# Optimization experiments

Hardware: AMD Instinct MI355X
Metric: run time of the kernel (lower is better)

## Reference

```python
import jax, jax.numpy as jnp
import numpy as np

B, C, H, W = 8, 256, 96, 96
HEADS, WS = 8, 12
HD = C // HEADS
SCALE = HD ** -0.5
L = WS * WS  # tokens per window


def _rel_index(ws):
    # Swin-style relative position index, computed statically (matches torch.meshgrid 'ij')
    coords = np.stack(np.meshgrid(np.arange(ws), np.arange(ws), indexing='ij')).reshape(2, -1)
    rel = (coords[:, :, None] - coords[:, None, :]).transpose(1, 2, 0) + (ws - 1)
    return rel[..., 0] * (2 * ws - 1) + rel[..., 1]  # [L, L]

REL_IDX = jnp.asarray(_rel_index(WS).reshape(-1))


def dct1(x):
    # 1D DCT-II along last axis via rfft, matches the torch implementation
    n = x.shape[-1]
    xv = jnp.concatenate([x, x[..., ::-1]], axis=-1)
    X = jnp.fft.rfft(xv, axis=-1)[..., :n]
    k = jnp.arange(n, dtype=jnp.float32)
    Wc = jnp.exp(-1j * jnp.pi * k / (2 * n))
    return (X * Wc).real.astype(jnp.float32)


def dct2(x):
    x = dct1(x.swapaxes(-1, -2)).swapaxes(-1, -2)
    return dct1(x)


def idct1(X):
    n = X.shape[-1]
    k = jnp.arange(n, dtype=jnp.float32)
    Wc = jnp.exp(1j * jnp.pi * k / (2 * n))
    Xc = X.astype(jnp.complex64) * Wc
    Xc_full = jnp.concatenate([Xc, Xc[..., 1:-1][..., ::-1]], axis=-1)
    # irfft with n=2n crops input to n+1 bins, exactly like torch.fft.irfft
    x = jnp.fft.irfft(Xc_full, n=2 * n, axis=-1)
    return x[..., :n].astype(jnp.float32)


def idct2(x):
    x = idct1(x.swapaxes(-1, -2)).swapaxes(-1, -2)
    return idct1(x)


def conv2d(x, w, groups=1, pad=0):
    return jax.lax.conv_general_dilated(
        x, w, (1, 1), [(pad, pad), (pad, pad)],
        dimension_numbers=('NCHW', 'OIHW', 'NCHW'), feature_group_count=groups)


def batchnorm(x, g, b):
    # training-mode BN (module default): per-batch statistics over (B,H,W)
    m = x.mean(axis=(0, 2, 3), keepdims=True)
    v = x.var(axis=(0, 2, 3), keepdims=True)
    return (x - m) * jax.lax.rsqrt(v + 1e-5) * g.reshape(1, -1, 1, 1) + b.reshape(1, -1, 1, 1)


def setup_inputs() -> dict:
    key = jax.random.key(0)
    ks = jax.random.split(key, 10)
    def rn(k, shape, s=0.02):
        return jax.random.normal(k, shape, dtype=jnp.float32) * s
    return {
        'x': jax.random.normal(ks[0], (B, C, H, W), dtype=jnp.float32),
        'qkv_w': rn(ks[1], (3 * C, C)), 'qkv_b': jnp.zeros((3 * C,), jnp.float32),
        'proj_w': rn(ks[2], (C, C)), 'proj_b': jnp.zeros((C,), jnp.float32),
        'lpe_w': rn(ks[3], (C, 1, 3, 3), 0.1), 'lpe_b': jnp.zeros((C,), jnp.float32),
        'lpe_scale': jnp.ones((1,), jnp.float32),
        'rpb_table': rn(ks[4], ((2 * WS - 1) ** 2, HEADS), 0.02),
        'ec_w': rn(ks[5], (1, 1, 3, 3), 0.3),
        'bn1_g': jnp.ones((1,), jnp.float32), 'bn1_b': jnp.zeros((1,), jnp.float32),
        'nl_w': rn(ks[6], (1, 1), 1.0), 'nl_b': jnp.zeros((1,), jnp.float32),
        'fr_w': rn(ks[7], (C, C, 1, 1), 0.05),
        'bn2_g': jnp.ones((C,), jnp.float32), 'bn2_b': jnp.zeros((C,), jnp.float32),
    }


def reference(x, qkv_w, qkv_b, proj_w, proj_b, lpe_w, lpe_b, lpe_scale, rpb_table,
              ec_w, bn1_g, bn1_b, nl_w, nl_b, fr_w, bn2_g, bn2_b):
    # ---- FreqNoiseDetector ----
    freq = jnp.abs(dct2(x))                                      # [B,C,H,W]
    mn = freq.min(axis=(2, 3), keepdims=True)
    mx = freq.max(axis=(2, 3), keepdims=True)
    freq_norm = (freq - mn) / (mx + 1e-6)
    local_energy = jax.nn.relu(batchnorm(
        conv2d(freq_norm.mean(axis=1, keepdims=True), ec_w, pad=1), bn1_g, bn1_b))  # [B,1,H,W]
    pooled = local_energy.mean(axis=(2, 3))                      # [B,1]
    noise_global = jax.nn.sigmoid(pooled @ nl_w.T + nl_b)        # [B,1]
    noise_mask = jax.nn.sigmoid(1.0 - local_energy) * noise_global.reshape(B, 1, 1, 1)

    # ---- DynamicAttention: SW-MSA with relative position bias ----
    xh = x.transpose(0, 2, 3, 1)                                 # [B,H,W,C]
    win = xh.reshape(B, H // WS, WS, W // WS, WS, C).transpose(0, 1, 3, 2, 4, 5).reshape(-1, L, C)
    qkv = (win @ qkv_w.T + qkv_b).reshape(-1, L, 3, HEADS, HD).transpose(2, 0, 3, 1, 4)
    q, k, v = qkv[0], qkv[1], qkv[2]                             # [Bw,h,L,hd]
    attn = jnp.einsum('bhld,bhmd->bhlm', q, k) * SCALE
    bias = rpb_table[REL_IDX].reshape(L, L, HEADS).transpose(2, 0, 1)
    attn = jax.nn.softmax(attn + bias[None], axis=-1)
    out = jnp.einsum('bhlm,bhmd->bhld', attn, v).transpose(0, 2, 1, 3).reshape(-1, L, C)
    out = out @ proj_w.T + proj_b
    x_attn = out.reshape(B, H // WS, W // WS, WS, WS, C).transpose(0, 1, 3, 2, 4, 5).reshape(B, H, W, C)
    # noise-guided depthwise LPE
    x_lpe = (conv2d(x, lpe_w, groups=C, pad=1) + lpe_b.reshape(1, C, 1, 1)) * lpe_scale * noise_mask
    x_attn_img = x_attn.transpose(0, 3, 1, 2) + x_lpe            # [B,C,H,W]

    # ---- frequency soft gate ----
    freq2 = dct2(x_attn_img)
    freq_mean = freq2.mean(axis=(2, 3), keepdims=True)
    gate = jax.nn.sigmoid(5.0 * (jnp.abs(freq2) - freq_mean))
    x_freq = idct2(freq2 * gate)

    # ---- 1x1 refine + residual ----
    y = batchnorm(conv2d(x + x_freq, fr_w), bn2_g, bn2_b)
    return jax.nn.gelu(y, approximate=False)
```

## Files before the change

### kernel.cpp

```cpp
#include <hip/hip_runtime.h>
#include <math.h>

#define Bb     8
#define Cc     256
#define Hh     96
#define Ww     96
#define HEADS  8
#define WS_    12
#define HD     32
#define LL     144
#define NPIX   9216
#define NPLANE 2048
#define NTOK   73728
#define NWIN   512
#define SCALE_ 0.17677669529663687f
#define BN1N   73728.0f
#define GELC   0.7071067811865476f

#define OFF_DT    0
#define OFF_FNM   18432
#define OFF_E     92160
#define OFF_MASK  165888
#define OFF_P3    239616
#define OFF_ST1   240192
#define OFF_BN2   240200
#define OFF_BUF0  262144
#define OFF_BUF1  19136512
#define OFF_BUF2  38010880

#define QKV_TSEC 4718592

typedef short bf16x8 __attribute__((ext_vector_type(8)));
typedef short s16x4  __attribute__((ext_vector_type(4)));
typedef float f32x4  __attribute__((ext_vector_type(4)));

static __device__ __forceinline__ float sigm(float x){ return 1.0f/(1.0f+__expf(-x)); }

static __device__ __forceinline__ void split2(float f, short& h, short& l){
  unsigned u = __float_as_uint(f);
  unsigned hb = u & 0xffff0000u;
  h = (short)(hb>>16);
  float lo = f - __uint_as_float(hb);
  l = (short)(__float_as_uint(lo)>>16);
}

__global__ void k_mat(short* DFh, short* DFl, short* MFh, short* MFl){
  int t = blockIdx.x*256 + threadIdx.x;
  int m = t/9216, u = t - m*9216;
  int k = u/96, n = u - k*96;
  double v;
  if (m == 0){
    v = 2.0*cos(3.14159265358979323846*(double)n*(double)(2*k+1)/192.0);
  } else {
    v = (k==0) ? 1.0 : 2.0*cos(3.14159265358979323846*(double)k*(double)(2*n+1)/192.0);
    if (k == 94) v += cos(3.14159265358979323846*94.0/192.0) * ((n&1)? -1.0 : 1.0);
    v /= 192.0;
  }
  float f = (float)v;
  short hs, ls; split2(f, hs, ls);
  int kt = k>>5, lr = (k>>3)&3, jj = k&7, nt = n>>4;
  int idx = ((kt*6+nt)*64 + (lr*16 + (n&15)))*8 + jj;
  if (m == 0){ DFh[idx]=hs; DFl[idx]=ls; }
  else       { MFh[idx]=hs; MFl[idx]=ls; }
}

__global__ __launch_bounds__(256) void k_plane(const float* __restrict__ in, float* __restrict__ out,
                                               const short* __restrict__ Fh, const short* __restrict__ Fl,
                                               int mode){
  __shared__ __align__(16) short Xh[96*104];
  __shared__ __align__(16) short Xl[96*104];
  __shared__ float red[512];
  const int tid = threadIdx.x;
  const int lane = tid & 63, wid = tid >> 6;
  const int l15 = lane & 15, l4 = lane >> 4;
  const float* src = in + (size_t)blockIdx.x*NPIX;

  for (int t4 = tid; t4 < 576; t4 += 256){
    int rt = t4/24, ct = t4 - rt*24;
    const float* p0 = src + rt*4*96 + ct*4;
    float4 v0 = *(const float4*)(p0);
    float4 v1 = *(const float4*)(p0+96);
    float4 v2 = *(const float4*)(p0+192);
    float4 v3 = *(const float4*)(p0+288);
#define STCOL(f0,f1,f2,f3,j) { s16x4 hv, lv; short hs, ls; \
    split2(f0,hs,ls); hv[0]=hs; lv[0]=ls; \
    split2(f1,hs,ls); hv[1]=hs; lv[1]=ls; \
    split2(f2,hs,ls); hv[2]=hs; lv[2]=ls; \
    split2(f3,hs,ls); hv[3]=hs; lv[3]=ls; \
    int cc = ct*4+(j); \
    *(s16x4*)&Xh[cc*104 + rt*4] = hv; \
    *(s16x4*)&Xl[cc*104 + rt*4] = lv; }
    STCOL(v0.x,v1.x,v2.x,v3.x,0)
    STCOL(v0.y,v1.y,v2.y,v3.y,1)
    STCOL(v0.z,v1.z,v2.z,v3.z,2)
    STCOL(v0.w,v1.w,v2.w,v3.w,3)
#undef STCOL
  }
  __syncthreads();

  f32x4 acc[9];
  #pragma unroll
  for (int t=0;t<9;++t) acc[t] = (f32x4){0.f,0.f,0.f,0.f};

  #pragma unroll
  for (int t=0;t<9;++t){
    int gt = wid*9 + t;
    int mt = gt/6, nt = gt - mt*6;
    int arow = mt*16 + l15;
    #pragma unroll
    for (int kb=0;kb<3;++kb){
      bf16x8 ah = *(const bf16x8*)&Xh[arow*104 + kb*32 + l4*8];
      bf16x8 al = *(const bf16x8*)&Xl[arow*104 + kb*32 + l4*8];
      const bf16x8 bh = *(const bf16x8*)(Fh + (size_t)((kb*6+nt)*64 + lane)*8);
      const bf16x8 bl = *(const bf16x8*)(Fl + (size_t)((kb*6+nt)*64 + lane)*8);
      acc[t] = __builtin_amdgcn_mfma_f32_16x16x32_bf16(al, bh, acc[t], 0,0,0);
      acc[t] = __builtin_amdgcn_mfma_f32_16x16x32_bf16(ah, bl, acc[t], 0,0,0);
      acc[t] = __builtin_amdgcn_mfma_f32_16x16x32_bf16(ah, bh, acc[t], 0,0,0);
    }
  }
  __syncthreads();

  #pragma unroll
  for (int t=0;t<9;++t){
    int gt = wid*9 + t;
    int mt = gt/6, nt = gt - mt*6;
    int ti = nt*16 + l15, tj = mt*16 + l4*4;
    s16x4 hv, lv; short hs, ls;
    split2(acc[t][0],hs,ls); hv[0]=hs; lv[0]=ls;
    split2(acc[t][1],hs,ls); hv[1]=hs; lv[1]=ls;
    split2(acc[t][2],hs,ls); hv[2]=hs; lv[2]=ls;
    split2(acc[t][3],hs,ls); hv[3]=hs; lv[3]=ls;
    *(s16x4*)&Xh[ti*104+tj] = hv;
    *(s16x4*)&Xl[ti*104+tj] = lv;
  }
  #pragma unroll
  for (int t=0;t<9;++t) acc[t] = (f32x4){0.f,0.f,0.f,0.f};
  __syncthreads();

  #pragma unroll
  for (int t=0;t<9;++t){
    int gt = wid*9 + t;
    int it = gt/6, jt = gt - it*6;
    int arow = it*16 + l15;
    #pragma unroll
    for (int kb=0;kb<3;++kb){
      bf16x8 ah = *(const bf16x8*)&Xh[arow*104 + kb*32 + l4*8];
// ... 58 lines not shown
      int i0 = it*16 + l4*4, j = jt*16 + l15;
      #pragma unroll
      for (int p=0;p<4;++p){
        float v = acc[t][p];
        dst[(i0+p)*96 + j] = v * sigm(5.f*(fabsf(v)-mean));
      }
    }
  }
}

__global__ void k_chmean(const float* __restrict__ A, float* __restrict__ FNM){
  int px = blockIdx.x*256 + threadIdx.x;
  int b = px/NPIX, p = px - b*NPIX;
  const float* base = A + (size_t)b*Cc*NPIX + p;
  float s = 0.f;
  #pragma unroll 8
  for (int c=0;c<Cc;++c) s += base[(size_t)c*NPIX];
  FNM[px] = s*(1.f/256.f);
}

__global__ void k_conv3(const float* __restrict__ FNM, const float* __restrict__ w9,
                        float* __restrict__ E, float* __restrict__ P3){
  __shared__ float rs[256], rq[256];
  int px = blockIdx.x*256 + threadIdx.x;
  int b = px/NPIX, p = px - b*NPIX;
  int h = p/96, w = p - h*96;
  const float* base = FNM + b*NPIX;
  float a = 0.f;
  #pragma unroll
  for (int dy=0;dy<3;++dy){
    int hh = h+dy-1;
    if (hh>=0 && hh<96){
      #pragma unroll
      for (int dx=0;dx<3;++dx){
        int ww2 = w+dx-1;
        if (ww2>=0 && ww2<96) a = fmaf(base[hh*96+ww2], w9[dy*3+dx], a);
      }
    }
  }
  E[px] = a;
  rs[threadIdx.x]=a; rq[threadIdx.x]=a*a; __syncthreads();
  for (int o=128;o;o>>=1){
    if (threadIdx.x<o){ rs[threadIdx.x]+=rs[threadIdx.x+o]; rq[threadIdx.x]+=rq[threadIdx.x+o]; }
    __syncthreads();
  }
  if (threadIdx.x==0){ P3[2*blockIdx.x]=rs[0]; P3[2*blockIdx.x+1]=rq[0]; }
}

__global__ void k_red576(const float* __restrict__ P3, float* __restrict__ ST1){
  __shared__ float rs[256], rq[256];
  float s=0.f,q=0.f;
  for (int i=threadIdx.x;i<288;i+=256){ s+=P3[2*i]; q+=P3[2*i+1]; }
  rs[threadIdx.x]=s; rq[threadIdx.x]=q; __syncthreads();
  for (int o=128;o;o>>=1){
    if (threadIdx.x<o){ rs[threadIdx.x]+=rs[threadIdx.x+o]; rq[threadIdx.x]+=rq[threadIdx.x+o]; }
    __syncthreads();
  }
  if (threadIdx.x==0){ ST1[0]=rs[0]; ST1[1]=rq[0]; }
}

__global__ void k_mask(const float* __restrict__ E, const float* __restrict__ ST1,
                       const float* __restrict__ g1, const float* __restrict__ b1,
                       const float* __restrict__ nw, const float* __restrict__ nb,
                       float* __restrict__ MASK){
  __shared__ float les[NPIX];
  __shared__ float red[256];
  int b = blockIdx.x, tid = threadIdx.x;
  float m = ST1[0]*(1.f/BN1N);
  float v = ST1[1]*(1.f/BN1N) - m*m;
  float rstd = rsqrtf(v + 1e-5f);
  float ga = g1[0], be = b1[0];
  float local = 0.f;
  for (int p=tid;p<NPIX;p+=256){
    float le = fmaxf(0.f, (E[b*NPIX+p]-m)*rstd*ga + be);
    les[p] = le; local += le;
  }
  red[tid]=local; __syncthreads();
  for (int o=128;o;o>>=1){ if (tid<o) red[tid]+=red[tid+o]; __syncthreads(); }
  float ng = sigm(red[0]*(1.f/9216.f)*nw[0] + nb[0]);
  for (int p=tid;p<NPIX;p+=256)
    MASK[b*NPIX+p] = sigm(1.f - les[p]) * ng;
}

__global__ void k_tr(const float* __restrict__ x, float* __restrict__ XT){
  __shared__ float tile[32][33];
  int pt = blockIdx.x*32, ct = blockIdx.y*32, b = blockIdx.z;
  int txd = threadIdx.x, tyd = threadIdx.y;
  #pragma unroll
  for (int q=0;q<4;++q){
    int c = ct + tyd + q*8;
    tile[tyd+q*8][txd] = x[(size_t)(b*Cc+c)*NPIX + pt + txd];
  }
  __syncthreads();
  #pragma unroll
  for (int q=0;q<4;++q){
    int p = pt + tyd + q*8;
    XT[(size_t)(b*NPIX+p)*Cc + ct + txd] = tile[txd][tyd+q*8];
  }
}

__global__ __launch_bounds__(256) void k_qkv(const float* __restrict__ XT, const float* __restrict__ Wq,
                                             const float* __restrict__ bq, float* __restrict__ qkv, int g){
  __shared__ __align__(16) float As[16*128];
  __shared__ __align__(16) float Bs[16*96];
  const int mt = blockIdx.x, nt = blockIdx.y;
  const int r0 = mt*128;
  const int tid = threadIdx.x;
  const int ty = tid>>4, tx = tid&15;
  float acc[8][6];
  #pragma unroll
  for (int a=0;a<8;++a){
    #pragma unroll
    for (int b=0;b<6;++b) acc[a][b]=0.f;
  }

  for (int k0=0;k0<256;k0+=16){
    #pragma unroll
    for (int it=0;it<2;++it){
      int f = tid + it*256;
      int i = f>>2, kq = f&3;
      int r = r0 + i;
      int win = r/144, l = r - win*144;
      int b = win>>6, wh = (win>>3)&7, wwi = win&7;
      int lh = l/12, lw = l - lh*12;
      int pix = (wh*12+lh)*96 + wwi*12+lw;
      float4 v = *(const float4*)&XT[((size_t)((b*NPIX)+pix))*256 + k0 + (kq<<2)];
      int kk = kq<<2;
      As[(kk+0)*128+i]=v.x; As[(kk+1)*128+i]=v.y; As[(kk+2)*128+i]=v.z; As[(kk+3)*128+i]=v.w;
    }
    #pragma unroll
    for (int it=0;it<2;++it){
      int f = tid + it*256;
      if (f < 384){
        int c = f>>2, kq = f&3;
        int cg = nt*96 + c;
        int t = cg>>6, hl = (cg>>5)&1, d = cg&31;
        int wrow = t*256 + (g*2+hl)*32 + d;
        float4 v = *(const float4*)&Wq[(size_t)wrow*256 + k0 + (kq<<2)];
        int kk = kq<<2;
        Bs[(kk+0)*96+c]=v.x; Bs[(kk+1)*96+c]=v.y; Bs[(kk+2)*96+c]=v.z; Bs[(kk+3)*96+c]=v.w;
      }
    }
    __syncthreads();
    #pragma unroll
    for (int k=0;k<16;++k){
      const float4* pa = (const float4*)&As[k*128 + ty*8];
      float4 a0 = pa[0], a1 = pa[1];
      float av[8] = {a0.x,a0.y,a0.z,a0.w,a1.x,a1.y,a1.z,a1.w};
      const float2* pb = (const float2*)&Bs[k*96];
      float2 b0 = pb[tx], b1 = pb[tx+16], b2 = pb[tx+32];
      float bv[6] = {b0.x,b0.y,b1.x,b1.y,b2.x,b2.y};
      #pragma unroll
      for (int ii=0;ii<8;++ii){
        #pragma unroll
        for (int jj=0;jj<6;++jj) acc[ii][jj] = fmaf(av[ii], bv[jj], acc[ii][jj]);
      }
    }
    __syncthreads();
  }
  #pragma unroll
  for (int ii=0;ii<8;++ii){
    int r = r0 + ty*8 + ii;
    int win = r/144, l = r - win*144;
    #pragma unroll
    for (int jj=0;jj<6;++jj){
      int s = jj>>1;
      int c = nt*96 + 2*tx + s*32 + (jj&1);
      int t = c>>6, hl = (c>>5)&1, d = c&31;
      float val = acc[ii][jj] + bq[t*256 + (g*2+hl)*32 + d];
      qkv[(size_t)t*QKV_TSEC + ((size_t)(win*2+hl)*144 + l)*32 + d] = val;
    }
  }
}

__global__ __launch_bounds__(192) void k_attn(const float* __restrict__ qkv, const float* __restrict__ rpb,
                                              float* __restrict__ O, int g){
  __shared__ __align__(16) float qt[32*144];
  __shared__ __align__(16) float Ks[144*32];
  __shared__ __align__(16) float Vs[144*32];
  __shared__ float rpbs[532];
  const int win = blockIdx.x, hl = blockIdx.y;
  const int head = g*2 + hl;
  const int tid = threadIdx.x;
  const float* Qg = qkv + ((size_t)(win*2+hl)*144)*32;
  const float* Kg = Qg + QKV_TSEC;
  const float* Vg = Qg + 2*(size_t)QKV_TSEC;
  for (int t=tid; t<4608; t+=192){
    Ks[t] = Kg[t]; Vs[t] = Vg[t];
    int l = t>>5, d = t&31;
    qt[d*144+l] = Qg[t];
  }
  for (int t=tid; t<529; t+=192) rpbs[t] = rpb[t*8 + head];
  __syncthreads();

  int r = tid;
  if (r < 144){
    float q[32];
    #pragma unroll
    for (int d=0;d<32;++d) q[d] = qt[d*144+r];
    float o[32];
    #pragma unroll
    for (int d=0;d<32;++d) o[d]=0.f;
    float m = -3.4e38f, sum = 0.f;
    int rh = r/12, rw = r - rh*12;
    int jh = 0, jw = 0;
    for (int j=0;j<144;++j){
      const float4* kp = (const float4*)&Ks[j*32];
      float s0=0,s1=0,s2=0,s3=0;
      #pragma unroll
      for (int t=0;t<8;++t){
        float4 kv = kp[t];
        s0 = fmaf(q[4*t+0],kv.x,s0); s1 = fmaf(q[4*t+1],kv.y,s1);
        s2 = fmaf(q[4*t+2],kv.z,s2); s3 = fmaf(q[4*t+3],kv.w,s3);
      }
      float s = ((s0+s1)+(s2+s3))*SCALE_ + rpbs[(rh-jh+11)*23 + (rw-jw+11)];
      float mn2 = fmaxf(m, s);
      if (mn2 > m){
        float corr = __expf(m - mn2);
        sum *= corr;
        #pragma unroll
        for (int d=0;d<32;++d) o[d]*=corr;
        m = mn2;
      }
      float p = __expf(s - m);
      sum += p;
      const float4* vp = (const float4*)&Vs[j*32];
      #pragma unroll
      for (int t=0;t<8;++t){
        float4 vv = vp[t];
        o[4*t+0]=fmaf(p,vv.x,o[4*t+0]); o[4*t+1]=fmaf(p,vv.y,o[4*t+1]);
        o[4*t+2]=fmaf(p,vv.z,o[4*t+2]); o[4*t+3]=fmaf(p,vv.w,o[4*t+3]);
      }
      if (++jw==12){ jw=0; ++jh; }
    }
    float inv = 1.f/sum;
    float* dst = O + ((size_t)(win*144+r))*256 + head*32;
    #pragma unroll
    for (int t=0;t<8;++t){
      float4 t4 = { o[4*t]*inv, o[4*t+1]*inv, o[4*t+2]*inv, o[4*t+3]*inv };
      *(float4*)&dst[4*t] = t4;
    }
  }
}

__global__ void k_lpe(const float* __restrict__ x, const float* __restrict__ lw,
                      const float* __restrict__ lb, const float* __restrict__ ls,
                      const float* __restrict__ MASK, float* __restrict__ Y1){
  float scale = ls[0];
  for (size_t idx = (size_t)blockIdx.x*256 + threadIdx.x; idx < (size_t)Bb*Cc*NPIX; idx += (size_t)gridDim.x*256){
    int pc = (int)(idx/NPIX); int p = (int)(idx - (size_t)pc*NPIX);
    int b = pc>>8, c = pc&255;
    int h = p/96, w = p - h*96;
    const float* xp = x + (size_t)pc*NPIX;
    const float* wp = lw + c*9;
    float a = 0.f;
    #pragma unroll
    for (int dy=0;dy<3;++dy){
      int hh = h+dy-1;
      if (hh>=0 && hh<96){
        #pragma unroll
        for (int dx=0;dx<3;++dx){
          int ww2 = w+dx-1;
          if (ww2>=0 && ww2<96) a = fmaf(xp[hh*96+ww2], wp[dy*3+dx], a);
        }
      }
    }
    Y1[idx] += (a + lb[c]) * scale * MASK[b*NPIX+p];
  }
}

__global__ __launch_bounds__(256) void k_proj(const float* __restrict__ O, const float* __restrict__ Wp,
                                              const float* __restrict__ bp, float* __restrict__ PROJ){
  __shared__ __align__(16) float As[16*128];
  __shared__ __align__(16) float Bs[16*128];
  const int mt = blockIdx.x, nt = blockIdx.y;
  const int r0 = mt*128, c0 = nt*128;
  const int tid = threadIdx.x;
  const int ty = tid>>4, tx = tid&15;
  float acc[8][8];
  #pragma unroll
  for (int a=0;a<8;++a){
    #pragma unroll
    for (int b=0;b<8;++b) acc[a][b]=0.f;
  }

  for (int k0=0;k0<256;k0+=16){
    #pragma unroll
    for (int it=0;it<2;++it){
      int f = tid + it*256;
      int i = f>>2, kq = f&3;
      float4 v = *(const float4*)&O[((size_t)(r0+i))*256 + k0 + (kq<<2)];
      int kk = kq<<2;
      As[(kk+0)*128+i]=v.x; As[(kk+1)*128+i]=v.y; As[(kk+2)*128+i]=v.z; As[(kk+3)*128+i]=v.w;
    }
    #pragma unroll
    for (int it=0;it<2;++it){
      int f = tid + it*256;
      int c = f>>2, kq = f&3;
      float4 v = *(const float4*)&Wp[((size_t)(c0+c))*256 + k0 + (kq<<2)];
      int kk = kq<<2;
      Bs[(kk+0)*128+c]=v.x; Bs[(kk+1)*128+c]=v.y; Bs[(kk+2)*128+c]=v.z; Bs[(kk+3)*128+c]=v.w;
    }
    __syncthreads();
    #pragma unroll
    for (int k=0;k<16;++k){
      const float4* pa = (const float4*)&As[k*128 + ty*8];
      float4 a0 = pa[0], a1 = pa[1];
      float av[8] = {a0.x,a0.y,a0.z,a0.w,a1.x,a1.y,a1.z,a1.w};
      const float4* pb = (const float4*)&Bs[k*128];
      float4 b0 = pb[tx], b1 = pb[tx+16];
      float bv[8] = {b0.x,b0.y,b0.z,b0.w,b1.x,b1.y,b1.z,b1.w};
      #pragma unroll
      for (int ii=0;ii<8;++ii){
        #pragma unroll
        for (int jj=0;jj<8;++jj) acc[ii][jj] = fmaf(av[ii], bv[jj], acc[ii][jj]);
      }
    }
    __syncthreads();
  }
  const float4 bp0 = *(const float4*)&bp[c0 + 4*tx];
  const float4 bp1 = *(const float4*)&bp[c0 + 64 + 4*tx];
  #pragma unroll
  for (int ii=0;ii<8;++ii){
    int r = r0 + ty*8 + ii;
    float* pp = PROJ + (size_t)r*256 + c0;
    float4 v0 = { acc[ii][0]+bp0.x, acc[ii][1]+bp0.y, acc[ii][2]+bp0.z, acc[ii][3]+bp0.w };
    float4 v1 = { acc[ii][4]+bp1.x, acc[ii][5]+bp1.y, acc[ii][6]+bp1.z, acc[ii][7]+bp1.w };
    *(float4*)&pp[4*tx] = v0;
    *(float4*)&pp[64 + 4*tx] = v1;
  }
}

__global__ __launch_bounds__(256) void k_merge(const float* __restrict__ PROJ, float* __restrict__ Y1){
  __shared__ float T[96*65];
  const int bx = blockIdx.x;
  const int b = bx/96, h = bx - b*96;
  const int wh = h/12, lh = h - wh*12;
  const int c0 = blockIdx.y*64;
  const int t = threadIdx.x;
  const int wave = t>>6, lane = t&63;
  for (int it=0; it<24; ++it){
    int tok = wave*24 + it;
    int wwi = tok/12, lw = tok - wwi*12;
    int gtok = (b*64 + wh*8 + wwi)*144 + lh*12 + lw;
    T[tok*65 + lane] = PROJ[(size_t)gtok*256 + c0 + lane];
  }
  __syncthreads();
  const int cl = t>>2, p0 = (t&3)*24;
  float* dst = Y1 + ((size_t)(b*Cc + c0 + cl))*NPIX + h*96 + p0;
  #pragma unroll
  for (int i=0;i<24;i+=4){
    float4 v = { T[(p0+i)*65+cl], T[(p0+i+1)*65+cl], T[(p0+i+2)*65+cl], T[(p0+i+3)*65+cl] };
    *(float4*)&dst[i] = v;
  }
}

__global__ __launch_bounds__(256) void k_conv1x1(const float* __restrict__ x, const float* __restrict__ XF,
                                                 const float* __restrict__ Wf, float* __restrict__ Z){
  __shared__ __align__(16) float As[16*128];
  __shared__ __align__(16) float Bs[16*128];
  const int mt = blockIdx.x, nt = blockIdx.y;
  const int gp0 = mt*128;
  const int b = gp0/NPIX, p0 = gp0 - b*NPIX;
  const int c0 = nt*128;
  const int tid = threadIdx.x;
  const int ty = tid>>4, tx = tid&15;
  float acc[8][8];
  #pragma unroll
  for (int a=0;a<8;++a){
    #pragma unroll
    for (int bb=0;bb<8;++bb) acc[a][bb]=0.f;
  }

  for (int k0=0;k0<256;k0+=16){
    #pragma unroll
    for (int it=0;it<2;++it){
      int f = tid + it*256;
      int k = f>>5, i4 = f&31;
      size_t off = ((size_t)(b*Cc + k0 + k))*NPIX + p0 + i4*4;
      float4 va = *(const float4*)&x[off];
      float4 vb = *(const float4*)&XF[off];
      float4 s = { va.x+vb.x, va.y+vb.y, va.z+vb.z, va.w+vb.w };
      *(float4*)&As[k*128 + i4*4] = s;
    }
    #pragma unroll
    for (int it=0;it<2;++it){
      int f = tid + it*256;
      int c = f>>2, kq = f&3;
      float4 v = *(const float4*)&Wf[((size_t)(c0+c))*256 + k0 + (kq<<2)];
      int kk = kq<<2;
      Bs[(kk+0)*128+c]=v.x; Bs[(kk+1)*128+c]=v.y; Bs[(kk+2)*128+c]=v.z; Bs[(kk+3)*128+c]=v.w;
    }
    __syncthreads();
    #pragma unroll
    for (int k=0;k<16;++k){
      const float4* pa = (const float4*)&As[k*128 + ty*8];
      float4 a0 = pa[0], a1 = pa[1];
      float av[8] = {a0.x,a0.y,a0.z,a0.w,a1.x,a1.y,a1.z,a1.w};
      const float4* pb = (const float4*)&Bs[k*128];
      float4 b0 = pb[tx], b1 = pb[tx+16];
      float bv[8] = {b0.x,b0.y,b0.z,b0.w,b1.x,b1.y,b1.z,b1.w};
      #pragma unroll
      for (int ii=0;ii<8;++ii){
        #pragma unroll
        for (int jj=0;jj<8;++jj) acc[ii][jj] = fmaf(av[ii], bv[jj], acc[ii][jj]);
      }
    }
    __syncthreads();
  }
  #pragma unroll
  for (int jj=0;jj<8;++jj){
    int co = c0 + ((jj<4)? 4*tx+jj : 64 + 4*tx + (jj-4));
    float4 lo = {acc[0][jj],acc[1][jj],acc[2][jj],acc[3][jj]};
    float4 hi = {acc[4][jj],acc[5][jj],acc[6][jj],acc[7][jj]};
    float* zp = Z + ((size_t)(b*Cc+co))*NPIX + p0 + ty*8;
    *(float4*)zp = lo;
    *(float4*)(zp+4) = hi;
  }
}

__global__ void k_bnstat(const float* __restrict__ Z, float* __restrict__ BN2){
  __shared__ float rs[256], rq[256];
  int c = blockIdx.x, tid = threadIdx.x;
  float s=0.f,q=0.f;
  for (int b=0;b<Bb;++b){
    const float* pl = Z + ((size_t)(b*Cc+c))*NPIX;
    for (int i=tid;i<NPIX/4;i+=256){
      float4 v = *(const float4*)&pl[i*4];
      s += v.x+v.y+v.z+v.w;
      q += v.x*v.x + v.y*v.y + v.z*v.z + v.w*v.w;
    }
  }
  rs[tid]=s; rq[tid]=q; __syncthreads();
  for (int o=128;o;o>>=1){
    if (tid<o){ rs[tid]+=rs[tid+o]; rq[tid]+=rq[tid+o]; }
    __syncthreads();
  }
  if (tid==0){ BN2[c]=rs[0]; BN2[256+c]=rq[0]; }
}

__global__ void k_final(const float* __restrict__ Z, const float* __restrict__ BN2,
                        const float* __restrict__ g2, const float* __restrict__ b2,
                        float* __restrict__ out){
  size_t f4 = (size_t)blockIdx.x*256 + threadIdx.x;
  size_t base = f4*4;
  int c = (int)((base/NPIX) & 255);
  float m = BN2[c]*(1.f/BN1N);
  float v = BN2[256+c]*(1.f/BN1N) - m*m;
  float rstd = rsqrtf(v+1e-5f);
  float ga = g2[c], be = b2[c];
  float4 z = *(const float4*)&Z[base];
  float4 r;
  float y;
  y = (z.x-m)*rstd*ga + be; r.x = 0.5f*y*(1.f+erff(y*GELC));
  y = (z.y-m)*rstd*ga + be; r.y = 0.5f*y*(1.f+erff(y*GELC));
  y = (z.z-m)*rstd*ga + be; r.z = 0.5f*y*(1.f+erff(y*GELC));
  y = (z.w-m)*rstd*ga + be; r.w = 0.5f*y*(1.f+erff(y*GELC));
  *(float4*)&out[base] = r;
}

extern "C" void kernel_launch(void* const* d_in, const int* in_sizes, int n_in,
                              void* d_out, int out_size, void* d_ws, size_t ws_size,
                              hipStream_t stream){
  const float* x      = (const float*)d_in[0];
  const float* qkv_w  = (const float*)d_in[1];
  const float* qkv_b  = (const float*)d_in[2];
  const float* proj_w = (const float*)d_in[3];
  const float* proj_b = (const float*)d_in[4];
  const float* lpe_w  = (const float*)d_in[5];
  const float* lpe_b  = (const float*)d_in[6];
  const float* lpe_s  = (const float*)d_in[7];
  const float* rpb    = (const float*)d_in[8];
  const float* ec_w   = (const float*)d_in[9];
  const float* bn1_g  = (const float*)d_in[10];
  const float* bn1_b  = (const float*)d_in[11];
  const float* nl_w   = (const float*)d_in[12];
  const float* nl_b   = (const float*)d_in[13];
  const float* fr_w   = (const float*)d_in[14];
  const float* bn2_g  = (const float*)d_in[15];
  const float* bn2_b  = (const float*)d_in[16];
  float* outp = (float*)d_out;

  float* WS   = (float*)d_ws;
  short* FR   = (short*)(WS + OFF_DT);
  short* DFh  = FR;
  short* DFl  = FR + 9216;
  short* MFh  = FR + 18432;
  short* MFl  = FR + 27648;
  float* FNM  = WS + OFF_FNM;
  float* E    = WS + OFF_E;
  float* MASK = WS + OFF_MASK;
  float* P3   = WS + OFF_P3;
  float* ST1  = WS + OFF_ST1;
  float* BN2  = WS + OFF_BN2;
  float* BUF0 = WS + OFF_BUF0;
  float* BUF1 = WS + OFF_BUF1;
  float* BUF2 = WS + OFF_BUF2;

  k_mat<<<72,256,0,stream>>>(DFh, DFl, MFh, MFl);
  k_plane<<<NPLANE,256,0,stream>>>(x, BUF2, DFh, DFl, 0);
  k_chmean<<<288,256,0,stream>>>(BUF2, FNM);
  k_conv3<<<288,256,0,stream>>>(FNM, ec_w, E, P3);
  k_red576<<<1,256,0,stream>>>(P3, ST1);
  k_mask<<<8,256,0,stream>>>(E, ST1, bn1_g, bn1_b, nl_w, nl_b, MASK);
  k_tr<<<dim3(288,8,8),dim3(32,8),0,stream>>>(x, BUF0);
  for (int g=0; g<4; ++g){
    k_qkv<<<dim3(576,2),256,0,stream>>>(BUF0, qkv_w, qkv_b, BUF1, g);
    k_attn<<<dim3(512,2),192,0,stream>>>(BUF1, rpb, BUF2, g);
  }
  k_proj<<<dim3(576,2),256,0,stream>>>(BUF2, proj_w, proj_b, BUF0);
  k_merge<<<dim3(768,4),256,0,stream>>>(BUF0, BUF1);
  k_lpe<<<4096,256,0,stream>>>(x, lpe_w, lpe_b, lpe_s, MASK, BUF1);
  k_plane<<<NPLANE,256,0,stream>>>(BUF1, BUF2, DFh, DFl, 1);
  k_plane<<<NPLANE,256,0,stream>>>(BUF2, BUF0, MFh, MFl, 2);
  k_conv1x1<<<dim3(576,2),256,0,stream>>>(x, BUF0, fr_w, BUF1);
  k_bnstat<<<256,256,0,stream>>>(BUF1, BN2);
  k_final<<<18432,256,0,stream>>>(BUF1, BN2, bn2_g, bn2_b, outp);
}
```

Before: 1.828 ms.

## Move QKV, projection and 1x1 conv GEMMs to split-bf16 MFMA; fuse LPE into merge

Replaces the three FP32 SIMT GEMMs (QKV, output projection, 1x1 refine conv) with MFMA bf16 kernels that use a hi/lo split (three MFMAs per tile) to keep near-FP32 accuracy. Weights are pre-swizzled into MFMA fragment layout, and activations are split into bf16 pairs at the producer: the transpose now writes window-ordered tokens, and attention writes split output. The depthwise LPE conv is folded into the merge kernel, which removes a separate pass over the full tensor. Buffers are reused heavily, which risks aliasing mistakes, and the split costs some accuracy and extra operand traffic.

```diff
diff --git a/kernel.cpp b/kernel.cpp
--- a/kernel.cpp
+++ b/kernel.cpp
@@ -3,8 +3,6 @@
 
 #define Bb     8
 #define Cc     256
-#define Hh     96
-#define Ww     96
 #define HEADS  8
 #define WS_    12
 #define HD     32
@@ -29,6 +27,8 @@
 #define OFF_BUF2  38010880
 
 #define QKV_TSEC 4718592
+#define QF_OFF  14155776
+#define PF_OFF  14352384
 
 typedef short bf16x8 __attribute__((ext_vector_type(8)));
 typedef short s16x4  __attribute__((ext_vector_type(4)));
@@ -62,6 +62,31 @@
   int idx = ((kt*6+nt)*64 + (lr*16 + (n&15)))*8 + jj;
   if (m == 0){ DFh[idx]=hs; DFl[idx]=ls; }
   else       { MFh[idx]=hs; MFl[idx]=ls; }
+}
+
+__global__ void k_wfrag(const float* __restrict__ qw, const float* __restrict__ pw,
+                        short* QFh, short* QFl, short* PFh, short* PFl){
+  int t = blockIdx.x*256 + threadIdx.x;
+  if (t < 196608){
+    int wrow = t>>8, k = t&255;
+    int sec = wrow>>8, rem = wrow&255, head = rem>>5, d = rem&31;
+    int g = head>>1, hl = head&1;
+    int nl = sec*64 + hl*32 + d;
+    int idx = (((g*8 + (k>>5))*12 + (nl>>4))*64 + ((k>>3)&3)*16 + (nl&15))*8 + (k&7);
+    short h,l; split2(qw[t],h,l); QFh[idx]=h; QFl[idx]=l;
+  } else {
+    int u = t - 196608;
+    int n = u>>8, k = u&255;
+    int idx = (((k>>5)*16 + (n>>4))*64 + ((k>>3)&3)*16 + (n&15))*8 + (k&7);
+    short h,l; split2(pw[u],h,l); PFh[idx]=h; PFl[idx]=l;
+  }
+}
+
+__global__ void k_wfrag_fr(const float* __restrict__ fw, short* FFh, short* FFl){
+  int u = blockIdx.x*256 + threadIdx.x;
+  int n = u>>8, k = u&255;
+  int idx = (((k>>5)*16 + (n>>4))*64 + ((k>>3)&3)*16 + (n&15))*8 + (k&7);
+  short h,l; split2(fw[u],h,l); FFh[idx]=h; FFl[idx]=l;
 }
 
 __global__ __launch_bounds__(256) void k_plane(const float* __restrict__ in, float* __restrict__ out,
@@ -286,7 +311,7 @@
     MASK[b*NPIX+p] = sigm(1.f - les[p]) * ng;
 }
 
-__global__ void k_tr(const float* __restrict__ x, float* __restrict__ XT){
+__global__ void k_tr(const float* __restrict__ x, short* __restrict__ XTH, short* __restrict__ XTL){
   __shared__ float tile[32][33];
   int pt = blockIdx.x*32, ct = blockIdx.y*32, b = blockIdx.z;
   int txd = threadIdx.x, tyd = threadIdx.y;
@@ -299,86 +324,69 @@
   #pragma unroll
   for (int q=0;q<4;++q){
     int p = pt + tyd + q*8;
-    XT[(size_t)(b*NPIX+p)*Cc + ct + txd] = tile[txd][tyd+q*8];
-  }
-}
-
-__global__ __launch_bounds__(256) void k_qkv(const float* __restrict__ XT, const float* __restrict__ Wq,
-                                             const float* __restrict__ bq, float* __restrict__ qkv, int g){
-  __shared__ __align__(16) float As[16*128];
-  __shared__ __align__(16) float Bs[16*96];
-  const int mt = blockIdx.x, nt = blockIdx.y;
-  const int r0 = mt*128;
-  const int tid = threadIdx.x;
-  const int ty = tid>>4, tx = tid&15;
-  float acc[8][6];
-  #pragma unroll
-  for (int a=0;a<8;++a){
-    #pragma unroll
-    for (int b=0;b<6;++b) acc[a][b]=0.f;
-  }
-
-  for (int k0=0;k0<256;k0+=16){
-    #pragma unroll
-    for (int it=0;it<2;++it){
-      int f = tid + it*256;
-      int i = f>>2, kq = f&3;
-      int r = r0 + i;
-      int win = r/144, l = r - win*144;
-      int b = win>>6, wh = (win>>3)&7, wwi = win&7;
-      int lh = l/12, lw = l - lh*12;
-      int pix = (wh*12+lh)*96 + wwi*12+lw;
-      float4 v = *(const float4*)&XT[((size_t)((b*NPIX)+pix))*256 + k0 + (kq<<2)];
-      int kk = kq<<2;
-      As[(kk+0)*128+i]=v.x; As[(kk+1)*128+i]=v.y; As[(kk+2)*128+i]=v.z; As[(kk+3)*128+i]=v.w;
-    }
-    #pragma unroll
-    for (int it=0;it<2;++it){
-      int f = tid + it*256;
-      if (f < 384){
-        int c = f>>2, kq = f&3;
-        int cg = nt*96 + c;
-        int t = cg>>6, hl = (cg>>5)&1, d = cg&31;
-        int wrow = t*256 + (g*2+hl)*32 + d;
-        float4 v = *(const float4*)&Wq[(size_t)wrow*256 + k0 + (kq<<2)];
-        int kk = kq<<2;
-        Bs[(kk+0)*96+c]=v.x; Bs[(kk+1)*96+c]=v.y; Bs[(kk+2)*96+c]=v.z; Bs[(kk+3)*96+c]=v.w;
-      }
-    }
-    __syncthreads();
-    #pragma unroll
-    for (int k=0;k<16;++k){
-      const float4* pa = (const float4*)&As[k*128 + ty*8];
-      float4 a0 = pa[0], a1 = pa[1];
-      float av[8] = {a0.x,a0.y,a0.z,a0.w,a1.x,a1.y,a1.z,a1.w};
-      const float2* pb = (const float2*)&Bs[k*96];
-      float2 b0 = pb[tx], b1 = pb[tx+16], b2 = pb[tx+32];
-      float bv[6] = {b0.x,b0.y,b1.x,b1.y,b2.x,b2.y};
-      #pragma unroll
-      for (int ii=0;ii<8;++ii){
-        #pragma unroll
-        for (int jj=0;jj<6;++jj) acc[ii][jj] = fmaf(av[ii], bv[jj], acc[ii][jj]);
-      }
-    }
-    __syncthreads();
-  }
-  #pragma unroll
-  for (int ii=0;ii<8;++ii){
-    int r = r0 + ty*8 + ii;
-    int win = r/144, l = r - win*144;
-    #pragma unroll
-    for (int jj=0;jj<6;++jj){
-      int s = jj>>1;
-      int c = nt*96 + 2*tx + s*32 + (jj&1);
-      int t = c>>6, hl = (c>>5)&1, d = c&31;
-      float val = acc[ii][jj] + bq[t*256 + (g*2+hl)*32 + d];
-      qkv[(size_t)t*QKV_TSEC + ((size_t)(win*2+hl)*144 + l)*32 + d] = val;
+    int h = p/96, w = p - h*96;
+    int wh = h/12, lh = h - wh*12, wwi = w/12, lw = w - wwi*12;
+    int token = (b*64 + wh*8 + wwi)*144 + lh*12 + lw;
+    float v = tile[txd][tyd+q*8];
+    short hs, ls; split2(v, hs, ls);
+    XTH[(size_t)token*256 + ct + txd] = hs;
+    XTL[(size_t)token*256 + ct + txd] = ls;
+  }
+}
+
+__global__ __launch_bounds__(256) void k_qkvm(const short* __restrict__ XTH, const short* __restrict__ XTL,
+                                              const short* __restrict__ QFh, const short* __restrict__ QFl,
+                                              const float* __restrict__ bq, float* __restrict__ qkv, int g){
+  const int tid = threadIdx.x, lane = tid&63, wid = tid>>6;
+  const int l15 = lane&15, l4 = lane>>4;
+  const int M0 = blockIdx.x*128;
+  f32x4 acc[2][12];
+  #pragma unroll
+  for (int m=0;m<2;++m){
+    #pragma unroll
+    for (int n=0;n<12;++n) acc[m][n] = (f32x4){0.f,0.f,0.f,0.f};
+  }
+  for (int kb=0; kb<8; ++kb){
+    bf16x8 ah[2], al[2];
+    #pragma unroll
+    for (int m=0;m<2;++m){
+      size_t off = (size_t)(M0 + (2*wid+m)*16 + l15)*256 + kb*32 + l4*8;
+      ah[m] = *(const bf16x8*)(XTH + off);
+      al[m] = *(const bf16x8*)(XTL + off);
+    }
+    #pragma unroll
+    for (int nt=0; nt<12; ++nt){
+      const bf16x8 bh = *(const bf16x8*)(QFh + (size_t)(((g*8+kb)*12+nt)*64 + lane)*8);
+      const bf16x8 bl = *(const bf16x8*)(QFl + (size_t)(((g*8+kb)*12+nt)*64 + lane)*8);
+      #pragma unroll
+      for (int m=0;m<2;++m){
+        acc[m][nt] = __builtin_amdgcn_mfma_f32_16x16x32_bf16(al[m], bh, acc[m][nt], 0,0,0);
+        acc[m][nt] = __builtin_amdgcn_mfma_f32_16x16x32_bf16(ah[m], bl, acc[m][nt], 0,0,0);
+        acc[m][nt] = __builtin_amdgcn_mfma_f32_16x16x32_bf16(ah[m], bh, acc[m][nt], 0,0,0);
+      }
+    }
+  }
+  #pragma unroll
+  for (int m=0;m<2;++m){
+    int tok0 = M0 + (2*wid+m)*16 + l4*4;
+    int win[4], ll[4];
+    #pragma unroll
+    for (int p=0;p<4;++p){ int tk = tok0+p; win[p] = tk/144; ll[p] = tk - win[p]*144; }
+    #pragma unroll
+    for (int nt=0; nt<12; ++nt){
+      int n = nt*16 + l15;
+      int sec = n>>6, hl = (n>>5)&1, d = n&31;
+      float bias = bq[sec*256 + (g*2+hl)*32 + d];
+      #pragma unroll
+      for (int p=0;p<4;++p){
+        qkv[(size_t)sec*QKV_TSEC + ((size_t)(win[p]*2+hl)*144 + ll[p])*32 + d] = acc[m][nt][p] + bias;
+      }
     }
   }
 }
 
 __global__ __launch_bounds__(192) void k_attn(const float* __restrict__ qkv, const float* __restrict__ rpb,
-                                              float* __restrict__ O, int g){
+                                              short* __restrict__ OH, short* __restrict__ OL, int g){
   __shared__ __align__(16) float qt[32*144];
   __shared__ __align__(16) float Ks[144*32];
   __shared__ __align__(16) float Vs[144*32];
@@ -438,104 +446,73 @@
       if (++jw==12){ jw=0; ++jh; }
     }
     float inv = 1.f/sum;
-    float* dst = O + ((size_t)(win*144+r))*256 + head*32;
+    size_t base = ((size_t)(win*144+r))*256 + head*32;
     #pragma unroll
     for (int t=0;t<8;++t){
-      float4 t4 = { o[4*t]*inv, o[4*t+1]*inv, o[4*t+2]*inv, o[4*t+3]*inv };
-      *(float4*)&dst[4*t] = t4;
-    }
-  }
-}
-
-__global__ void k_lpe(const float* __restrict__ x, const float* __restrict__ lw,
-                      const float* __restrict__ lb, const float* __restrict__ ls,
-                      const float* __restrict__ MASK, float* __restrict__ Y1){
-  float scale = ls[0];
-  for (size_t idx = (size_t)blockIdx.x*256 + threadIdx.x; idx < (size_t)Bb*Cc*NPIX; idx += (size_t)gridDim.x*256){
-    int pc = (int)(idx/NPIX); int p = (int)(idx - (size_t)pc*NPIX);
-    int b = pc>>8, c = pc&255;
-    int h = p/96, w = p - h*96;
-    const float* xp = x + (size_t)pc*NPIX;
-    const float* wp = lw + c*9;
-    float a = 0.f;
-    #pragma unroll
-    for (int dy=0;dy<3;++dy){
-      int hh = h+dy-1;
-      if (hh>=0 && hh<96){
-        #pragma unroll
-        for (int dx=0;dx<3;++dx){
-          int ww2 = w+dx-1;
-          if (ww2>=0 && ww2<96) a = fmaf(xp[hh*96+ww2], wp[dy*3+dx], a);
-        }
-      }
-    }
-    Y1[idx] += (a + lb[c]) * scale * MASK[b*NPIX+p];
-  }
-}
-
-__global__ __launch_bounds__(256) void k_proj(const float* __restrict__ O, const float* __restrict__ Wp,
-                                              const float* __restrict__ bp, float* __restrict__ PROJ){
-  __shared__ __align__(16) float As[16*128];
-  __shared__ __align__(16) float Bs[16*128];
-  const int mt = blockIdx.x, nt = blockIdx.y;
-  const int r0 = mt*128, c0 = nt*128;
-  const int tid = threadIdx.x;
-  const int ty = tid>>4, tx = tid&15;
-  float acc[8][8];
-  #pragma unroll
-  for (int a=0;a<8;++a){
-    #pragma unroll
-    for (int b=0;b<8;++b) acc[a][b]=0.f;
-  }
-
-  for (int k0=0;k0<256;k0+=16){
-    #pragma unroll
-    for (int it=0;it<2;++it){
-      int f = tid + it*256;
-      int i = f>>2, kq = f&3;
-      float4 v = *(const float4*)&O[((size_t)(r0+i))*256 + k0 + (kq<<2)];
-      int kk = kq<<2;
-      As[(kk+0)*128+i]=v.x; As[(kk+1)*128+i]=v.y; As[(kk+2)*128+i]=v.z; As[(kk+3)*128+i]=v.w;
-    }
-    #pragma unroll
-    for (int it=0;it<2;++it){
-      int f = tid + it*256;
-      int c = f>>2, kq = f&3;
-      float4 v = *(const float4*)&Wp[((size_t)(c0+c))*256 + k0 + (kq<<2)];
-      int kk = kq<<2;
-      Bs[(kk+0)*128+c]=v.x; Bs[(kk+1)*128+c]=v.y; Bs[(kk+2)*128+c]=v.z; Bs[(kk+3)*128+c]=v.w;
-    }
-    __syncthreads();
-    #pragma unroll
-    for (int k=0;k<16;++k){
-      const float4* pa = (const float4*)&As[k*128 + ty*8];
-      float4 a0 = pa[0], a1 = pa[1];
-      float av[8] = {a0.x,a0.y,a0.z,a0.w,a1.x,a1.y,a1.z,a1.w};
-      const float4* pb = (const float4*)&Bs[k*128];
-      float4 b0 = pb[tx], b1 = pb[tx+16];
-      float bv[8] = {b0.x,b0.y,b0.z,b0.w,b1.x,b1.y,b1.z,b1.w};
-      #pragma unroll
-      for (int ii=0;ii<8;++ii){
-        #pragma unroll
-        for (int jj=0;jj<8;++jj) acc[ii][jj] = fmaf(av[ii], bv[jj], acc[ii][jj]);
-      }
-    }
-    __syncthreads();
-  }
-  const float4 bp0 = *(const float4*)&bp[c0 + 4*tx];
-  const float4 bp1 = *(const float4*)&bp[c0 + 64 + 4*tx];
-  #pragma unroll
-  for (int ii=0;ii<8;++ii){
-    int r = r0 + ty*8 + ii;
-    float* pp = PROJ + (size_t)r*256 + c0;
-    float4 v0 = { acc[ii][0]+bp0.x, acc[ii][1]+bp0.y, acc[ii][2]+bp0.z, acc[ii][3]+bp0.w };
-    float4 v1 = { acc[ii][4]+bp1.x, acc[ii][5]+bp1.y, acc[ii][6]+bp1.z, acc[ii][7]+bp1.w };
-    *(float4*)&pp[4*tx] = v0;
-    *(float4*)&pp[64 + 4*tx] = v1;
-  }
-}
-
-__global__ __launch_bounds__(256) void k_merge(const float* __restrict__ PROJ, float* __restrict__ Y1){
+      s16x4 hv, lv; short hs, ls;
+      split2(o[4*t+0]*inv,hs,ls); hv[0]=hs; lv[0]=ls;
+      split2(o[4*t+1]*inv,hs,ls); hv[1]=hs; lv[1]=ls;
+      split2(o[4*t+2]*inv,hs,ls); hv[2]=hs; lv[2]=ls;
+      split2(o[4*t+3]*inv,hs,ls); hv[3]=hs; lv[3]=ls;
+      *(s16x4*)&OH[base + 4*t] = hv;
+      *(s16x4*)&OL[base + 4*t] = lv;
+    }
+  }
+}
+
+__global__ __launch_bounds__(256) void k_projm(const short* __restrict__ OH, const short* __restrict__ OL,
+                                               const short* __restrict__ PFh, const short* __restrict__ PFl,
+                                               const float* __restrict__ bp, float* __restrict__ PROJ){
+  const int tid = threadIdx.x, lane = tid&63, wid = tid>>6;
+  const int l15 = lane&15, l4 = lane>>4;
+  const int M0 = blockIdx.x*128;
+  const int N0 = blockIdx.y*128;
+  f32x4 acc[2][8];
+  #pragma unroll
+  for (int m=0;m<2;++m){
+    #pragma unroll
+    for (int n=0;n<8;++n) acc[m][n] = (f32x4){0.f,0.f,0.f,0.f};
+  }
+  for (int kb=0; kb<8; ++kb){
+    bf16x8 ah[2], al[2];
+    #pragma unroll
+    for (int m=0;m<2;++m){
+      size_t off = (size_t)(M0 + (2*wid+m)*16 + l15)*256 + kb*32 + l4*8;
+      ah[m] = *(const bf16x8*)(OH + off);
+      al[m] = *(const bf16x8*)(OL + off);
+    }
+    #pragma unroll
+    for (int nt=0; nt<8; ++nt){
+      int ntg = (N0>>4) + nt;
+      const bf16x8 bh = *(const bf16x8*)(PFh + (size_t)((kb*16+ntg)*64 + lane)*8);
+      const bf16x8 bl = *(const bf16x8*)(PFl + (size_t)((kb*16+ntg)*64 + lane)*8);
+      #pragma unroll
+      for (int m=0;m<2;++m){
+        acc[m][nt] = __builtin_amdgcn_mfma_f32_16x16x32_bf16(al[m], bh, acc[m][nt], 0,0,0);
+        acc[m][nt] = __builtin_amdgcn_mfma_f32_16x16x32_bf16(ah[m], bl, acc[m][nt], 0,0,0);
+        acc[m][nt] = __builtin_amdgcn_mfma_f32_16x16x32_bf16(ah[m], bh, acc[m][nt], 0,0,0);
+      }
+    }
+  }
+  #pragma unroll
+  for (int m=0;m<2;++m){
+    int tok0 = M0 + (2*wid+m)*16 + l4*4;
+    #pragma unroll
+    for (int nt=0; nt<8; ++nt){
+      int n = N0 + nt*16 + l15;
+      float bias = bp[n];
+      #pragma unroll
+      for (int p=0;p<4;++p){
+        PROJ[(size_t)(tok0+p)*256 + n] = acc[m][nt][p] + bias;
+      }
+    }
+  }
+}
+
+__global__ __launch_bounds__(256) void k_merge(const float* __restrict__ PROJ, const float* __restrict__ x,
+                                               const float* __restrict__ lpw, const float* __restrict__ lpb,
+                                               const float* __restrict__ lps, const float* __restrict__ MASK,
+                                               float* __restrict__ Y1){
   __shared__ float T[96*65];
   const int bx = blockIdx.x;
   const int b = bx/96, h = bx - b*96;
@@ -545,81 +522,105 @@
   const int wave = t>>6, lane = t&63;
   for (int it=0; it<24; ++it){
     int tok = wave*24 + it;
-    int wwi = tok/12, lw = tok - wwi*12;
-    int gtok = (b*64 + wh*8 + wwi)*144 + lh*12 + lw;
+    int wwi = tok/12, lw2 = tok - wwi*12;
+    int gtok = (b*64 + wh*8 + wwi)*144 + lh*12 + lw2;
     T[tok*65 + lane] = PROJ[(size_t)gtok*256 + c0 + lane];
   }
   __syncthreads();
-  const int cl = t>>2, p0 = (t&3)*24;
-  float* dst = Y1 + ((size_t)(b*Cc + c0 + cl))*NPIX + h*96 + p0;
+  const int cl = t>>2, q = t&3, p0 = q*24;
+  const int c = c0 + cl;
+  const float* xc = x + (size_t)(b*Cc + c)*NPIX;
+  const float* wp = lpw + c*9;
+  float w0=wp[0],w1=wp[1],w2=wp[2],w3=wp[3],w4=wp[4],w5=wp[5],w6=wp[6],w7=wp[7],w8=wp[8];
+  float bias = lpb[c], scale = lps[0];
+  const float* mrow = MASK + b*NPIX + h*96;
+  const float* r0 = xc + (h-1)*96;
+  const float* r1 = xc + h*96;
+  const float* r2 = xc + (h+1)*96;
+  bool h0 = (h>0), h2 = (h<95);
+  float outv[24];
+  #pragma unroll 4
+  for (int i=0;i<24;++i){
+    int w = p0 + i;
+    bool wl = (w>0), wr = (w<95);
+    float a = 0.f;
+    if (h0){
+      if (wl) a = fmaf(r0[w-1],w0,a);
+      a = fmaf(r0[w],w1,a);
+      if (wr) a = fmaf(r0[w+1],w2,a);
+    }
+    if (wl) a = fmaf(r1[w-1],w3,a);
+    a = fmaf(r1[w],w4,a);
+    if (wr) a = fmaf(r1[w+1],w5,a);
+    if (h2){
+      if (wl) a = fmaf(r2[w-1],w6,a);
+      a = fmaf(r2[w],w7,a);
+      if (wr) a = fmaf(r2[w+1],w8,a);
+    }
+    outv[i] = (a + bias)*scale*mrow[w];
+  }
+  float* dst = Y1 + (size_t)(b*Cc + c)*NPIX + h*96 + p0;
   #pragma unroll
   for (int i=0;i<24;i+=4){
-    float4 v = { T[(p0+i)*65+cl], T[(p0+i+1)*65+cl], T[(p0+i+2)*65+cl], T[(p0+i+3)*65+cl] };
+    float4 v = { T[(p0+i)*65+cl]+outv[i], T[(p0+i+1)*65+cl]+outv[i+1],
+                 T[(p0+i+2)*65+cl]+outv[i+2], T[(p0+i+3)*65+cl]+outv[i+3] };
     *(float4*)&dst[i] = v;
   }
 }
 
-__global__ __launch_bounds__(256) void k_conv1x1(const float* __restrict__ x, const float* __restrict__ XF,
-                                                 const float* __restrict__ Wf, float* __restrict__ Z){
-  __shared__ __align__(16) float As[16*128];
-  __shared__ __align__(16) float Bs[16*128];
-  const int mt = blockIdx.x, nt = blockIdx.y;
-  const int gp0 = mt*128;
-  const int b = gp0/NPIX, p0 = gp0 - b*NPIX;
-  const int c0 = nt*128;
-  const int tid = threadIdx.x;
-  const int ty = tid>>4, tx = tid&15;
-  float acc[8][8];
-  #pragma unroll
-  for (int a=0;a<8;++a){
-    #pragma unroll
-    for (int bb=0;bb<8;++bb) acc[a][bb]=0.f;
-  }
-
-  for (int k0=0;k0<256;k0+=16){
-    #pragma unroll
-    for (int it=0;it<2;++it){
-      int f = tid + it*256;
-      int k = f>>5, i4 = f&31;
-      size_t off = ((size_t)(b*Cc + k0 + k))*NPIX + p0 + i4*4;
-      float4 va = *(const float4*)&x[off];
-      float4 vb = *(const float4*)&XF[off];
-      float4 s = { va.x+vb.x, va.y+vb.y, va.z+vb.z, va.w+vb.w };
-      *(float4*)&As[k*128 + i4*4] = s;
-    }
-    #pragma unroll
-    for (int it=0;it<2;++it){
-      int f = tid + it*256;
-      int c = f>>2, kq = f&3;
-      float4 v = *(const float4*)&Wf[((size_t)(c0+c))*256 + k0 + (kq<<2)];
-      int kk = kq<<2;
-      Bs[(kk+0)*128+c]=v.x; Bs[(kk+1)*128+c]=v.y; Bs[(kk+2)*128+c]=v.z; Bs[(kk+3)*128+c]=v.w;
+__global__ __launch_bounds__(256) void k_conv1x1m(const float* __restrict__ x, const float* __restrict__ XF,
+                                                  const short* __restrict__ FFh, const short* __restrict__ FFl,
+                                                  float* __restrict__ Z){
+  __shared__ __align__(16) short Ah[64*40];
+  __shared__ __align__(16) short Al[64*40];
+  const int tid = threadIdx.x, lane = tid&63, wid = tid>>6;
+  const int l15 = lane&15, l4 = lane>>4;
+  const int g0 = blockIdx.x*64;
+  const int b = g0/NPIX, p0 = g0 - b*NPIX;
+  f32x4 acc[16];
+  #pragma unroll
+  for (int n=0;n<16;++n) acc[n] = (f32x4){0.f,0.f,0.f,0.f};
+
+  for (int kb=0; kb<8; ++kb){
+    if (kb) __syncthreads();
+    if (tid < 128){
+      int cq = tid>>4, pq = tid&15;
+      float vv[4][4];
+      #pragma unroll
+      for (int j=0;j<4;++j){
+        size_t off = (size_t)(b*Cc + kb*32 + cq*4 + j)*NPIX + p0 + pq*4;
+        float4 va = *(const float4*)&x[off];
+        float4 vb = *(const float4*)&XF[off];
+        vv[j][0]=va.x+vb.x; vv[j][1]=va.y+vb.y; vv[j][2]=va.z+vb.z; vv[j][3]=va.w+vb.w;
+      }
+      #pragma unroll
+      for (int j2=0;j2<4;++j2){
+        s16x4 hv, lv; short hs, ls;
+        split2(vv[0][j2],hs,ls); hv[0]=hs; lv[0]=ls;
+        split2(vv[1][j2],hs,ls); hv[1]=hs; lv[1]=ls;
+        split2(vv[2][j2],hs,ls); hv[2]=hs; lv[2]=ls;
+        split2(vv[3][j2],hs,ls); hv[3]=hs; lv[3]=ls;
+        *(s16x4*)&Ah[(pq*4+j2)*40 + cq*4] = hv;
+        *(s16x4*)&Al[(pq*4+j2)*40 + cq*4] = lv;
+      }
     }
     __syncthreads();
-    #pragma unroll
-    for (int k=0;k<16;++k){
-      const float4* pa = (const float4*)&As[k*128 + ty*8];
-      float4 a0 = pa[0], a1 = pa[1];
-      float av[8] = {a0.x,a0.y,a0.z,a0.w,a1.x,a1.y,a1.z,a1.w};
-      const float4* pb = (const float4*)&Bs[k*128];
-      float4 b0 = pb[tx], b1 = pb[tx+16];
-      float bv[8] = {b0.x,b0.y,b0.z,b0.w,b1.x,b1.y,b1.z,b1.w};
-      #pragma unroll
-      for (int ii=0;ii<8;++ii){
-        #pragma unroll
-        for (int jj=0;jj<8;++jj) acc[ii][jj] = fmaf(av[ii], bv[jj], acc[ii][jj]);
-      }
-    }
-    __syncthreads();
-  }
-  #pragma unroll
-  for (int jj=0;jj<8;++jj){
-    int co = c0 + ((jj<4)? 4*tx+jj : 64 + 4*tx + (jj-4));
-    float4 lo = {acc[0][jj],acc[1][jj],acc[2][jj],acc[3][jj]};
-    float4 hi = {acc[4][jj],acc[5][jj],acc[6][jj],acc[7][jj]};
-    float* zp = Z + ((size_t)(b*Cc+co))*NPIX + p0 + ty*8;
-    *(float4*)zp = lo;
-    *(float4*)(zp+4) = hi;
+    bf16x8 ah = *(const bf16x8*)&Ah[(wid*16+l15)*40 + l4*8];
+    bf16x8 al = *(const bf16x8*)&Al[(wid*16+l15)*40 + l4*8];
+    #pragma unroll
+    for (int nt=0; nt<16; ++nt){
+      const bf16x8 bh = *(const bf16x8*)(FFh + (size_t)((kb*16+nt)*64 + lane)*8);
+      const bf16x8 bl = *(const bf16x8*)(FFl + (size_t)((kb*16+nt)*64 + lane)*8);
+      acc[nt] = __builtin_amdgcn_mfma_f32_16x16x32_bf16(al, bh, acc[nt], 0,0,0);
+      acc[nt] = __builtin_amdgcn_mfma_f32_16x16x32_bf16(ah, bl, acc[nt], 0,0,0);
+      acc[nt] = __builtin_amdgcn_mfma_f32_16x16x32_bf16(ah, bh, acc[nt], 0,0,0);
+    }
+  }
+  #pragma unroll
+  for (int nt=0; nt<16; ++nt){
+    int cch = nt*16 + l15;
+    float* zp = Z + (size_t)(b*Cc + cch)*NPIX + p0 + wid*16 + l4*4;
+    *(f32x4*)zp = acc[nt];
   }
 }
 
@@ -686,11 +687,10 @@
   float* outp = (float*)d_out;
 
   float* WS   = (float*)d_ws;
-  short* FR   = (short*)(WS + OFF_DT);
-  short* DFh  = FR;
-  short* DFl  = FR + 9216;
-  short* MFh  = FR + 18432;
-  short* MFl  = FR + 27648;
+  short* DFh  = (short*)(WS + OFF_DT);
+  short* DFl  = DFh + 9216;
+  short* MFh  = DFh + 18432;
+  short* MFl  = DFh + 27648;
   float* FNM  = WS + OFF_FNM;
   float* E    = WS + OFF_E;
   float* MASK = WS + OFF_MASK;
@@ -701,23 +701,44 @@
   float* BUF1 = WS + OFF_BUF1;
   float* BUF2 = WS + OFF_BUF2;
 
+  short* XTH = (short*)BUF0;
+  short* XTL = XTH + 18874368;
+  float* PROJ = BUF0;
+  float* XF   = BUF0;
+
+  float* QKV = BUF1;
+  short* QFh = (short*)(BUF1 + QF_OFF);
+  short* QFl = QFh + 196608;
+  short* PFh = (short*)(BUF1 + PF_OFF);
+  short* PFl = PFh + 65536;
+  float* Y1  = BUF1;
+  float* Zb  = BUF1;
+
+  float* A2  = BUF2;
+  short* OH  = (short*)BUF2;
+  short* OL  = OH + 18874368;
+  float* G   = BUF2;
+  short* FFh = (short*)BUF2;
+  short* FFl = FFh + 65536;
+
   k_mat<<<72,256,0,stream>>>(DFh, DFl, MFh, MFl);
-  k_plane<<<NPLANE,256,0,stream>>>(x, BUF2, DFh, DFl, 0);
-  k_chmean<<<288,256,0,stream>>>(BUF2, FNM);
+  k_wfrag<<<1024,256,0,stream>>>(qkv_w, proj_w, QFh, QFl, PFh, PFl);
+  k_plane<<<NPLANE,256,0,stream>>>(x, A2, DFh, DFl, 0);
+  k_chmean<<<288,256,0,stream>>>(A2, FNM);
   k_conv3<<<288,256,0,stream>>>(FNM, ec_w, E, P3);
   k_red576<<<1,256,0,stream>>>(P3, ST1);
   k_mask<<<8,256,0,stream>>>(E, ST1, bn1_g, bn1_b, nl_w, nl_b, MASK);
-  k_tr<<<dim3(288,8,8),dim3(32,8),0,stream>>>(x, BUF0);
+  k_tr<<<dim3(288,8,8),dim3(32,8),0,stream>>>(x, XTH, XTL);
   for (int g=0; g<4; ++g){
-    k_qkv<<<dim3(576,2),256,0,stream>>>(BUF0, qkv_w, qkv_b, BUF1, g);
-    k_attn<<<dim3(512,2),192,0,stream>>>(BUF1, rpb, BUF2, g);
-  }
-  k_proj<<<dim3(576,2),256,0,stream>>>(BUF2, proj_w, proj_b, BUF0);
-  k_merge<<<dim3(768,4),256,0,stream>>>(BUF0, BUF1);
-  k_lpe<<<4096,256,0,stream>>>(x, lpe_w, lpe_b, lpe_s, MASK, BUF1);
-  k_plane<<<NPLANE,256,0,stream>>>(BUF1, BUF2, DFh, DFl, 1);
-  k_plane<<<NPLANE,256,0,stream>>>(BUF2, BUF0, MFh, MFl, 2);
-  k_conv1x1<<<dim3(576,2),256,0,stream>>>(x, BUF0, fr_w, BUF1);
-  k_bnstat<<<256,256,0,stream>>>(BUF1, BN2);
-  k_final<<<18432,256,0,stream>>>(BUF1, BN2, bn2_g, bn2_b, outp);
-}
+    k_qkvm<<<576,256,0,stream>>>(XTH, XTL, QFh, QFl, qkv_b, QKV, g);
+    k_attn<<<dim3(512,2),192,0,stream>>>(QKV, rpb, OH, OL, g);
+  }
+  k_projm<<<dim3(576,2),256,0,stream>>>(OH, OL, PFh, PFl, proj_b, PROJ);
+  k_merge<<<dim3(768,4),256,0,stream>>>(PROJ, x, lpe_w, lpe_b, lpe_s, MASK, Y1);
+  k_plane<<<NPLANE,256,0,stream>>>(Y1, G, DFh, DFl, 1);
+  k_plane<<<NPLANE,256,0,stream>>>(G, XF, MFh, MFl, 2);
+  k_wfrag_fr<<<256,256,0,stream>>>(fr_w, FFh, FFl);
+  k_conv1x1m<<<1152,256,0,stream>>>(x, XF, FFh, FFl, Zb);
+  k_bnstat<<<256,256,0,stream>>>(Zb, BN2);
+  k_final<<<18432,256,0,stream>>>(Zb, BN2, bn2_g, bn2_b, outp);
+}
```

Measured after the change: 2.385 ms. 30.5% more time.
